# Performance work log

Measured on AMD Instinct MI355X. Metric: run time of the kernel, lower is better.

Reference implementation:

```python
import jax, jax.numpy as jnp
import numpy as np

S, B, T, H, K, FH, OUT = 4, 256, 256, 128, 5, 48, 1
DW, AW = 64, 32            # dynamics-MLP width, attention width
EPS_BN, EPS_U = 1e-5, 1e-6


def setup_inputs() -> dict:
    key = jax.random.key(0)
    ks = jax.random.split(key, 16)
    r = lambda i, shape, s: jax.random.normal(ks[i], shape, jnp.float32) * s
    return {
        "x": jax.random.normal(ks[0], (B, 1, T), jnp.float32),
        "t_span": jnp.linspace(0.0, 1.0, T, dtype=jnp.float32),
        # decomposer: per-scale DynamicDilationConv + BN + ReLU + Conv1d + BN + ReLU
        "c1w": r(1, (S, 1, 1, K), 0.3), "c1b": jnp.zeros((S, 1)),
        "bn1_g": jnp.ones((S, 1)), "bn1_b": jnp.zeros((S, 1)),
        "c2w": r(2, (S, 1, 1, K), 0.3), "c2b": jnp.zeros((S, 1)),
        "bn2_g": jnp.ones((S, 1)), "bn2_b": jnp.zeros((S, 1)),
        # per-scale ProbabilisticNeuralDynamics MLP: (H+1+1) -> 64 -> 2H
        "dw1": r(3, (S, H + 2, DW), 0.1), "db1": jnp.zeros((S, DW)),
        "dw2": r(4, (S, DW, 2 * H), 0.1), "db2": jnp.zeros((S, 2 * H)),
        # fusion attention H -> 32 -> 1
        "a1w": r(5, (H, AW), 0.1), "a1b": jnp.zeros((AW,)),
        "a2w": r(6, (AW, 1), 0.1), "a2b": jnp.zeros((1,)),
        # GRU (torch layout: W_ih [3H, in], W_hh [3H, H])
        "wih": r(7, (3 * H, OUT), 0.1), "whh": r(8, (3 * H, H), 0.05),
        "bih": jnp.zeros((3 * H,)), "bhh": jnp.zeros((3 * H,)),
        "fcw": r(9, (H, OUT), 0.1), "fcb": jnp.zeros((OUT,)),
        "lvw": r(10, (H, OUT), 0.1), "lvb": jnp.zeros((OUT,)),
        "init_token": jnp.zeros((1, OUT)),
    }


def _conv1d(x, w, b):
    # x:[B,C,L], w:[O,I,K]; dilation = round(clamp(exp(log_dilation=0),1)) = 1
    pad = (w.shape[-1] - 1) // 2
    y = jax.lax.conv_general_dilated(x, w, (1,), [(pad, pad)],
                                     dimension_numbers=("NCH", "OIH", "NCH"))
    return y + b[None, :, None]


def _bn(x, g, b):
    # BatchNorm1d in training mode: batch stats over (N, L)
    m = x.mean(axis=(0, 2), keepdims=True)
    v = x.var(axis=(0, 2), keepdims=True)
    return g[None, :, None] * (x - m) * jax.lax.rsqrt(v + EPS_BN) + b[None, :, None]


def _decompose(x, c1w, c1b, g1, b1, c2w, c2b, g2, b2):
    h = jnp.maximum(_bn(_conv1d(x, c1w, c1b), g1, b1), 0.0)
    h = jnp.maximum(_bn(_conv1d(h, c2w, c2b), g2, b2), 0.0)
    return h  # [B,1,T]


def _ode_scale(xseq, t_span, w1, b1, w2, b2):
    # xseq:[B,T,1]; integrate (mu, logvar) with RK4 on the t_span grid
    def f(t, h):
        idx = jnp.argmin(jnp.abs(t_span - t))
        x_t = jnp.take(xseq, idx, axis=1)                 # [B,1]
        tf = t * jnp.ones((h.shape[0], 1), h.dtype)       # time feature
        u = jnp.maximum(jnp.concatenate([h, x_t, tf], -1) @ w1 + b1, 0.0) @ w2 + b2
        return u[:, :H], u[:, H:]

    def step(carry, ts):
        h, lv = carry
        t0, t1 = ts
        dt = t1 - t0
        k1m, k1v = f(t0, h)
        k2m, k2v = f(t0 + dt / 2, h + dt / 2 * k1m)
        k3m, k3v = f(t0 + dt / 2, h + dt / 2 * k2m)
        k4m, k4v = f(t1, h + dt * k3m)
        h = h + dt / 6 * (k1m + 2 * k2m + 2 * k3m + k4m)
        lv = lv + dt / 6 * (k1v + 2 * k2v + 2 * k3v + k4v)
        return (h, lv), None

    z = jnp.zeros((xseq.shape[0], H), xseq.dtype)
    (h, lv), _ = jax.lax.scan(step, (z, z), (t_span[:-1], t_span[1:]))
    return h, lv  # final-time latent, matching h_sol[:, -1, :]


def _forward(x, t_span, c1w, c1b, bn1_g, bn1_b, c2w, c2b, bn2_g, bn2_b,
             dw1, db1, dw2, db2, a1w, a1b, a2w, a2b,
             wih, whh, bih, bhh, fcw, fcb, lvw, lvb, init_token):
    # multi-scale decomposition -> [S,B,1,T]
    comps = jax.vmap(_decompose, in_axes=(None, 0, 0, 0, 0, 0, 0, 0, 0))(
        x, c1w, c1b, bn1_g, bn1_b, c2w, c2b, bn2_g, bn2_b)
    xseqs = comps[:, :, 0, :, None]                       # [S,B,T,1]
    means, logvars = jax.vmap(_ode_scale, in_axes=(0, None, 0, 0, 0, 0))(
        xseqs, t_span, dw1, db1, dw2, db2)                # each [S,B,H]
    means = jnp.transpose(means, (1, 0, 2))               # [B,S,H]
    logvars = jnp.transpose(logvars, (1, 0, 2))
    # uncertainty-scaled attention fusion
    scores = jnp.maximum(means @ a1w + a1b, 0.0) @ a2w + a2b        # [B,S,1]
    uncert = jnp.mean(jnp.exp(logvars), axis=-1, keepdims=True)     # [B,S,1]
    weights = jax.nn.softmax(scores / (uncert + EPS_U), axis=1)
    fused = jnp.sum(weights * means, axis=1)              # [B,H]

    def dec_step(carry, _):
        h, tok = carry
        gi = tok @ wih.T + bih
        gh = h @ whh.T + bhh
        ir, iz, inn = jnp.split(gi, 3, axis=-1)
        hr, hz, hn = jnp.split(gh, 3, axis=-1)
        r = jax.nn.sigmoid(ir + hr)
        zz = jax.nn.sigmoid(iz + hz)
        n = jnp.tanh(inn + r * hn)
        h = (1.0 - zz) * n + zz * h
        pred = h @ fcw + fcb
        plv = h @ lvw + lvb
        return (h, pred), (pred, plv)

    tok0 = jnp.broadcast_to(init_token, (fused.shape[0], OUT))
    _, (outs, lvs) = jax.lax.scan(dec_step, (fused, tok0), None, length=FH)
    return jnp.transpose(outs, (1, 0, 2)), jnp.transpose(lvs, (1, 0, 2))


def reference(x, t_span, c1w, c1b, bn1_g, bn1_b, c2w, c2b, bn2_g, bn2_b,
              dw1, db1, dw2, db2, a1w, a1b, a2w, a2b,
              wih, whh, bih, bhh, fcw, fcb, lvw, lvb, init_token):
    return _forward(x, t_span, c1w, c1b, bn1_g, bn1_b, c2w, c2b, bn2_g, bn2_b,
                    dw1, db1, dw2, db2, a1w, a1b, a2w, a2b,
                    wih, whh, bih, bhh, fcw, fcb, lvw, lvb, init_token)
```

## Files before the change

### kernel.cpp

```cpp
#include <hip/hip_runtime.h>
#include <math.h>

#define NS   4
#define NB   256
#define NT   256
#define NH   128
#define NDW  64
#define NFH  48

__global__ __launch_bounds__(256) void k_d1(
    const float* __restrict__ x,
    const float* __restrict__ c1w, const float* __restrict__ c1b,
    float* __restrict__ tmpA, double* __restrict__ pp1)
{
    const int s     = blockIdx.x >> 6;
    const int chunk = blockIdx.x & 63;
    const int tid   = threadIdx.x;
    __shared__ double wred[4][2];

    float w[5];
#pragma unroll
    for (int k = 0; k < 5; ++k) w[k] = c1w[s*5 + k];
    const float cb = c1b[s];

    double ls = 0.0, lq = 0.0;
#pragma unroll
    for (int r = 0; r < 4; ++r) {
        const int bb = chunk*4 + r;
        const float* xb = x + bb*NT;
        float acc = cb;
#pragma unroll
        for (int k = 0; k < 5; ++k) {
            int tt = tid + k - 2;
            if (tt >= 0 && tt < NT) acc += xb[tt] * w[k];
        }
        tmpA[s*65536 + bb*NT + tid] = acc;
        ls += (double)acc; lq += (double)acc * (double)acc;
    }
#pragma unroll
    for (int off = 32; off > 0; off >>= 1) {
        ls += __shfl_xor(ls, off); lq += __shfl_xor(lq, off);
    }
    if ((tid & 63) == 0) { wred[tid>>6][0] = ls; wred[tid>>6][1] = lq; }
    __syncthreads();
    if (tid == 0) {
        pp1[(s*64 + chunk)*2 + 0] = wred[0][0]+wred[1][0]+wred[2][0]+wred[3][0];
        pp1[(s*64 + chunk)*2 + 1] = wred[0][1]+wred[1][1]+wred[2][1]+wred[3][1];
    }
}

__global__ __launch_bounds__(256) void k_d3(
    const float* __restrict__ tmpA, const double* __restrict__ pp1,
    const float* __restrict__ g1,  const float* __restrict__ b1,
    const float* __restrict__ c2w, const float* __restrict__ c2b,
    float* __restrict__ cv2, double* __restrict__ pp2)
{
    const int s     = blockIdx.x >> 6;
    const int chunk = blockIdx.x & 63;
    const int tid   = threadIdx.x;
    __shared__ float hsh[256];
    __shared__ double wred[4][2];

    double lsum = 0.0, lsq = 0.0;
    for (int q = 0; q < 64; ++q) {
        lsum += pp1[(s*64 + q)*2 + 0];
        lsq  += pp1[(s*64 + q)*2 + 1];
    }
    const double Nn = 65536.0;
    double mm = lsum / Nn;
    double vv = lsq / Nn - mm*mm;
    const float m1 = (float)mm, rs1 = (float)(1.0 / sqrt(vv + 1e-5));
    const float A1 = g1[s]*rs1, B1 = b1[s] - g1[s]*m1*rs1;

    float w[5];
#pragma unroll
    for (int k = 0; k < 5; ++k) w[k] = c2w[s*5 + k];
    const float cb = c2b[s];

    double ls = 0.0, lq = 0.0;
    for (int r = 0; r < 4; ++r) {
        const int bb = chunk*4 + r;
        float y = tmpA[s*65536 + bb*NT + tid];
        hsh[tid] = fmaxf(fmaf(A1, y, B1), 0.f);
        __syncthreads();
        float acc = cb;
#pragma unroll
        for (int k = 0; k < 5; ++k) {
            int tt = tid + k - 2;
            if (tt >= 0 && tt < NT) acc += hsh[tt] * w[k];
        }
        cv2[s*65536 + bb*NT + tid] = acc;
        ls += (double)acc; lq += (double)acc * (double)acc;
        __syncthreads();
    }
#pragma unroll
    for (int off = 32; off > 0; off >>= 1) {
        ls += __shfl_xor(ls, off); lq += __shfl_xor(lq, off);
    }
    if ((tid & 63) == 0) { wred[tid>>6][0] = ls; wred[tid>>6][1] = lq; }
    __syncthreads();
    if (tid == 0) {
        pp2[(s*64 + chunk)*2 + 0] = wred[0][0]+wred[1][0]+wred[2][0]+wred[3][0];
        pp2[(s*64 + chunk)*2 + 1] = wred[0][1]+wred[1][1]+wred[2][1]+wred[3][1];
    }
}

__global__ __launch_bounds__(64) void k_mat(
    const float* __restrict__ dw1, const float* __restrict__ dw2,
    const float* __restrict__ db2, const float* __restrict__ tspan,
    float* __restrict__ Mt, float* __restrict__ bM,
    int* __restrict__ imid_g, float* __restrict__ Tg)
{
    if (blockIdx.x == 256) {
        __shared__ float ts[256];
        const int t = threadIdx.x;
        for (int e = t; e < 256; e += 64) ts[e] = tspan[e];
        __syncthreads();
        for (int i = t; i < 255; i += 64) {
            float t0 = ts[i], t1 = ts[i+1];
            float tm = t0 + (t1 - t0) * 0.5f;
            int best = 0; float bd = fabsf(ts[0] - tm);
            for (int j = 1; j < 256; ++j) {
                float d = fabsf(ts[j] - tm);
                if (d < bd) { bd = d; best = j; }
            }
            imid_g[i] = best;
        }
        if (t == 0) {
            float T = 0.f;
            for (int i = 0; i < 255; ++i) T += (ts[i+1] - ts[i]);
            Tg[0] = T;
        }
        return;
    }
    const int s = blockIdx.x >> 6;
    const int c = blockIdx.x & 63;
    const int k = threadIdx.x;
    __shared__ float col[128];

    col[k]      = dw1[(s*130 + k)*64 + c];
    col[k + 64] = dw1[(s*130 + 64 + k)*64 + c];
    __syncthreads();

    const float4* dp = (const float4*)(dw2 + (s*64 + k)*256);
    double acc = 0.0;
#pragma unroll 8
    for (int j4 = 0; j4 < 32; ++j4) {
        float4 dv = dp[j4];
        acc += (double)dv.x * (double)col[4*j4+0]
             + (double)dv.y * (double)col[4*j4+1]
             + (double)dv.z * (double)col[4*j4+2]
             + (double)dv.w * (double)col[4*j4+3];
    }
    const int slot = (k & 48) | (((c & 15) - (k & 15)) & 15);
    Mt[(s*64 + c)*64 + slot] = (float)acc;

    double pb = (double)db2[s*256 + k]      * (double)col[k]
              + (double)db2[s*256 + 64 + k] * (double)col[k + 64];
#pragma unroll
    for (int off = 32; off > 0; off >>= 1) pb += __shfl_xor(pb, off);
    if (k == 0) bM[s*64 + c] = (float)pb;
}

__device__ __forceinline__ float rlf(float v, int l) {
    return __int_as_float(__builtin_amdgcn_readlane(__float_as_int(v), l));
}
__device__ __forceinline__ float pick4f(float r0, float r1, float r2, float r3, int i) {
    int l = i & 63, h = i >> 6;
    float a = (h & 2) ? ((h & 1) ? r3 : r2) : ((h & 1) ? r1 : r0);
    return rlf(a, l);
}
__device__ __forceinline__ float bperm(int addr, float v) {
    return __int_as_float(__builtin_amdgcn_ds_bpermute(addr, __float_as_int(v)));
}

#define FSTEP2(p) \
    asm("v_fmac_f32 %0, %1, %2 row_ror:" #p " row_mask:0xf bank_mask:0xf" \
        : "+v"(d0) : "v"(u0), "v"(McL[p])); \
    asm("v_fmac_f32 %0, %1, %2 row_ror:" #p " row_mask:0xf bank_mask:0xf" \
        : "+v"(d1) : "v"(u1v), "v"(McL[16+(p)]));

#define DOT(uin, vout) { \
    float u0 = bperm(A0, (uin)), u1v = bperm(A1, (uin)); \
    float d0 = fmaf(u0, McL[0], seed); \
    float d1 = u1v * McL[16]; \
    FSTEP2(1)  FSTEP2(2)  FSTEP2(3)  FSTEP2(4)  FSTEP2(5)  FSTEP2(6) \
    FSTEP2(7)  FSTEP2(8)  FSTEP2(9)  FSTEP2(10) FSTEP2(11) FSTEP2(12) \
    FSTEP2(13) FSTEP2(14) FSTEP2(15) \
    float part = d0 + d1; \
    pp[pb][w][l] = part; \
    __syncthreads(); \
    float oth = pp[pb][1 - w][l]; \
    vout = part + oth; \
    pb ^= 1; }

__global__ __attribute__((amdgpu_waves_per_eu(2)))
__launch_bounds__(128) void k_ode(
    const float* __restrict__ cv2, const double* __restrict__ pp2g,
    const float* __restrict__ g2,  const float* __restrict__ b2,
    const float* __restrict__ tspan, const int* __restrict__ imid_g,
    const float* __restrict__ Mt, const float* __restrict__ bM_g,
    const float* __restrict__ dw1, const float* __restrict__ db1,
    float* __restrict__ S_g)
{
    const int b   = blockIdx.x;
    const int s   = b >> 8;
    const int row = b & 255;
    const int tid = threadIdx.x;
    const int w   = tid >> 6;
    const int l   = tid & 63;

    __shared__ __align__(16) float xls[256];
    __shared__ __align__(16) float xms[256];
    __shared__ __align__(16) float pp[2][2][64];

    double lsum = 0.0, lsq = 0.0;
    for (int q = 0; q < 64; ++q) {
        lsum += pp2g[(s*64 + q)*2 + 0];
        lsq  += pp2g[(s*64 + q)*2 + 1];
    }
    const double Nn = 65536.0;
    double mmv = lsum / Nn;
    double vvv = lsq / Nn - mmv*mmv;
    const float m2 = (float)mmv, rs2 = (float)(1.0 / sqrt(vvv + 1e-5));
    const float bnA = g2[s]*rs2, bnB = b2[s] - g2[s]*m2*rs2;

    const float* __restrict__ xrow = cv2 + (s*NB + row)*NT;
    for (int e = tid; e < 256; e += 128)
        xls[e] = fmaxf(fmaf(bnA, xrow[e], bnB), 0.f);
    __syncthreads();
    for (int e = tid; e < 255; e += 128)
        xms[e] = xls[imid_g[e]];

    const float bMc = bM_g[s*64 + l];
    const float b1c = db1[s*64 + l];
    const float w1x = dw1[(s*130 + 128)*64 + l];
    const float w1t = dw1[(s*130 + 129)*64 + l];
    const float seed = (w == 0) ? bMc : 0.0f;

    float tr0 = tspan[l],       tr1 = tspan[64 + l];
    float tr2 = tspan[128 + l], tr3 = tspan[192 + l];

    float McL[32];
    const float4* mp = (const float4*)(Mt + (s*64 + l)*64 + 32*w);
#pragma unroll
    for (int j = 0; j < 8; ++j) {
        float4 t = mp[j];
        McL[4*j+0] = t.x; McL[4*j+1] = t.y; McL[4*j+2] = t.z; McL[4*j+3] = t.w;
    }
#pragma unroll
    for (int j = 0; j < 32; ++j) asm volatile("" : "+v"(McL[j]));

    const int lm = (l & 15) << 2;
    const int A0 = lm + 128*w;
    const int A1 = lm + 64 + 128*w;

    __syncthreads();

    float a = 0.f, S = 0.f;
    float t0  = rlf(tr0, 0);
    float t1  = rlf(tr0, 1);
    float xi  = xls[0], xmv = xms[0], x1v = xls[1];
    int   pb  = 0;

    for (int i = 0; i < 255; ++i) {
        float xin = 0.f, xmn = 0.f, x1n = 0.f, t1n = 0.f;
        if (i < 254) {
            xin = xls[i+1]; xmn = xms[i+1]; x1n = xls[i+2];
            t1n = pick4f(tr0, tr1, tr2, tr3, i + 2);
        }
        const float dt  = t1 - t0;
        const float tm  = t0 + dt * 0.5f;
        const float hdt = dt * 0.5f;
        const float c0  = b1c + xi*w1x  + t0*w1t;
        const float cm  = b1c + xmv*w1x + tm*w1t;
        const float c1  = b1c + x1v*w1x + t1*w1t;

        float u11 = fmaxf(a + c0, 0.f);
        float v1;  DOT(u11, v1)
        float u12 = fmaxf(fmaf(hdt, v1, a) + cm, 0.f);
        float v2;  DOT(u12, v2)
        float u13 = fmaxf(fmaf(hdt, v2, a) + cm, 0.f);
        float v3;  DOT(u13, v3)
        float u14 = fmaxf(fmaf(dt, v3, a) + c1, 0.f);
        float v4;  DOT(u14, v4)

        float d6 = dt * (1.0f / 6.0f);
        a += d6 * ((v1 + v4) + 2.f*(v2 + v3));
        S += d6 * ((u11 + u14) + 2.f*(u12 + u13));

        t0 = t1; t1 = t1n; xi = xin; xmv = xmn; x1v = x1n;
    }

    if (w == 0) S_g[(s*256 + row)*64 + l] = S;
}

__global__ __launch_bounds__(384, 1) void k_gru(
    const float* __restrict__ S_g, const float* __restrict__ dw2,
    const float* __restrict__ db2, const float* __restrict__ Tg,
    const float* __restrict__ a1w, const float* __restrict__ a1b,
    const float* __restrict__ a2w, const float* __restrict__ a2b,
    const float* __restrict__ wih, const float* __restrict__ whh,
    const float* __restrict__ bih, const float* __restrict__ bhh,
    const float* __restrict__ fcw, const float* __restrict__ fcb,
    const float* __restrict__ lvw, const float* __restrict__ lvb,
    const float* __restrict__ init_token, float* __restrict__ out)
{
    const int b   = blockIdx.x;
    const int tid = threadIdx.x;

    __shared__ __align__(16) float Ssh[4][64];
    __shared__ __align__(16) float msh[4][128];
    __shared__ __align__(16) float evs[4][128];
    __shared__ __align__(16) float hl[128];
    __shared__ float ghl[384];
    __shared__ float scoreL[4];
    __shared__ float unc_part[2][4];
    __shared__ float wgt[4];
    __shared__ float redL[2][2];
    __shared__ float tokL;

    if (tid < 256) {
        int s = tid >> 6, cc = tid & 63;
        Ssh[s][cc] = S_g[(s*256 + b)*64 + cc];
    }
    const float T = Tg[0];
    __syncthreads();

    for (int e = tid; e < 1024; e += 384) {
        int s = e >> 8, j = e & 255;
        float acc = T * db2[s*256 + j];
        const float4* s4 = (const float4*)Ssh[s];
#pragma unroll
        for (int k4 = 0; k4 < 16; ++k4) {
            float4 sv = s4[k4];
            acc += sv.x * dw2[(s*64 + 4*k4 + 0)*256 + j]
                 + sv.y * dw2[(s*64 + 4*k4 + 1)*256 + j]
                 + sv.z * dw2[(s*64 + 4*k4 + 2)*256 + j]
                 + sv.w * dw2[(s*64 + 4*k4 + 3)*256 + j];
        }
        if (j < 128) msh[s][j] = acc;
        else         evs[s][j - 128] = expf(acc);
    }
    __syncthreads();

    if (tid < 128) {
        int wv = tid >> 6;
#pragma unroll
        for (int s = 0; s < 4; ++s) {
            float v = evs[s][tid];
#pragma unroll
            for (int off = 32; off > 0; off >>= 1) v += __shfl_xor(v, off);
            if ((tid & 63) == 0) unc_part[wv][s] = v;
        }
    }
    if (tid < 128) {
        int s = tid >> 5, aq = tid & 31;
        float hd = a1b[aq];
#pragma unroll 4
        for (int i = 0; i < 128; ++i) hd += msh[s][i] * a1w[i*32 + aq];
        hd = fmaxf(hd, 0.f);
        float sc = hd * a2w[aq];
#pragma unroll
        for (int off = 16; off > 0; off >>= 1) sc += __shfl_xor(sc, off);
        if (aq == 0) scoreL[s] = sc + a2b[0];
    }
    __syncthreads();
    if (tid == 0) {
        float sv[4], mx = -1e30f;
#pragma unroll
        for (int s = 0; s < 4; ++s) {
            float u = (unc_part[0][s] + unc_part[1][s]) / 128.f;
            sv[s] = scoreL[s] / (u + 1e-6f);
            mx = fmaxf(mx, sv[s]);
        }
        float se = 0.f, ev[4];
#pragma unroll
        for (int s = 0; s < 4; ++s) { ev[s] = expf(sv[s] - mx); se += ev[s]; }
#pragma unroll
        for (int s = 0; s < 4; ++s) wgt[s] = ev[s] / se;
        tokL = init_token[0];
    }
    __syncthreads();
    if (tid < 128) {
        float f = 0.f;
#pragma unroll
        for (int s = 0; s < 4; ++s) f += wgt[s] * msh[s][tid];
        hl[tid] = f;
    }

    float4 whh4[32];
    const float4* wr = (const float4*)(whh + tid*128);
#pragma unroll
    for (int k = 0; k < 32; ++k) whh4[k] = wr[k];
    float bhhj = bhh[tid];
    float wih_r = 0.f, wih_z = 0.f, wih_n = 0.f;
    float bih_r = 0.f, bih_z = 0.f, bih_n = 0.f;
    float fcwi = 0.f, lvwi = 0.f;
    if (tid < 128) {
        wih_r = wih[tid]; wih_z = wih[128+tid]; wih_n = wih[256+tid];
        bih_r = bih[tid]; bih_z = bih[128+tid]; bih_n = bih[256+tid];
        fcwi  = fcw[tid]; lvwi  = lvw[tid];
    }
    const float fcbv = fcb[0], lvbv = lvb[0];
    __syncthreads();

    for (int t = 0; t < NFH; ++t) {
        float g0 = 0.f, g1 = 0.f, g2 = 0.f, g3 = 0.f;
        const float4* h4 = (const float4*)hl;
#pragma unroll
        for (int k = 0; k < 32; ++k) {
            float4 hv = h4[k];
            float4 wvv = whh4[k];
            g0 += hv.x * wvv.x; g1 += hv.y * wvv.y;
            g2 += hv.z * wvv.z; g3 += hv.w * wvv.w;
        }
        ghl[tid] = ((g0 + g1) + (g2 + g3)) + bhhj;
        __syncthreads();

        if (tid < 128) {
            float tok = tokL;
            float r  = 1.f / (1.f + expf(-(tok*wih_r + bih_r + ghl[tid])));
            float zz = 1.f / (1.f + expf(-(tok*wih_z + bih_z + ghl[128+tid])));
            float n  = tanhf(tok*wih_n + bih_n + r * ghl[256+tid]);
            float hn = (1.f - zz) * n + zz * hl[tid];
            hl[tid] = hn;
            float pg = hn * fcwi, pl = hn * lvwi;
#pragma unroll
            for (int off = 32; off > 0; off >>= 1) {
                pg += __shfl_xor(pg, off);
                pl += __shfl_xor(pl, off);
            }
            int wvx = tid >> 6;
            if ((tid & 63) == 0) { redL[wvx][0] = pg; redL[wvx][1] = pl; }
        }
        __syncthreads();
        if (tid == 0) {
            float pr = redL[0][0] + redL[1][0] + fcbv;
            float pv = redL[0][1] + redL[1][1] + lvbv;
            out[b*NFH + t] = pr;
            out[NB*NFH + b*NFH + t] = pv;
            tokL = pr;
        }
        __syncthreads();
    }
}

extern "C" void kernel_launch(void* const* d_in, const int* in_sizes, int n_in,
                              void* d_out, int out_size, void* d_ws, size_t ws_size,
                              hipStream_t stream)
{
    const float* x      = (const float*)d_in[0];
    const float* tspan  = (const float*)d_in[1];
    const float* c1w    = (const float*)d_in[2];
    const float* c1b    = (const float*)d_in[3];
    const float* bn1g   = (const float*)d_in[4];
    const float* bn1b   = (const float*)d_in[5];
    const float* c2w    = (const float*)d_in[6];
    const float* c2b    = (const float*)d_in[7];
    const float* bn2g   = (const float*)d_in[8];
    const float* bn2b   = (const float*)d_in[9];
    const float* dw1    = (const float*)d_in[10];
    const float* db1    = (const float*)d_in[11];
    const float* dw2    = (const float*)d_in[12];
    const float* db2    = (const float*)d_in[13];
    const float* a1w    = (const float*)d_in[14];
    const float* a1b    = (const float*)d_in[15];
    const float* a2w    = (const float*)d_in[16];
    const float* a2b    = (const float*)d_in[17];
    const float* wih    = (const float*)d_in[18];
    const float* whh    = (const float*)d_in[19];
    const float* bih    = (const float*)d_in[20];
    const float* bhh    = (const float*)d_in[21];
    const float* fcw    = (const float*)d_in[22];
    const float* fcb    = (const float*)d_in[23];
    const float* lvw    = (const float*)d_in[24];
    const float* lvb    = (const float*)d_in[25];
    const float* itok   = (const float*)d_in[26];

    float* ws    = (float*)d_ws;
    float*  cv2  = ws;
    float*  tmpA = ws + 262144;
    float*  S_g  = ws + 524288;
    float*  Mt   = ws + 589824;
    float*  bMg  = ws + 606208;
    float*  Tg   = ws + 606464;
    int*    imid = (int*)(ws + 606720);
    double* pp1  = (double*)(ws + 606976);
    double* pp2  = (double*)(ws + 608000);

    k_d1<<<256, 256, 0, stream>>>(x, c1w, c1b, tmpA, pp1);
    k_mat<<<257, 64, 0, stream>>>(dw1, dw2, db2, tspan, Mt, bMg, imid, Tg);
    k_d3<<<256, 256, 0, stream>>>(tmpA, pp1, bn1g, bn1b, c2w, c2b, cv2, pp2);
    k_ode<<<1024, 128, 0, stream>>>(cv2, pp2, bn2g, bn2b, tspan, imid,
                                    Mt, bMg, dw1, db1, S_g);
    k_gru<<<256, 384, 0, stream>>>(S_g, dw2, db2, Tg, a1w, a1b, a2w, a2b,
                                   wih, whh, bih, bhh, fcw, fcb, lvw, lvb,
                                   itok, (float*)d_out);
}
```

Baseline: 406.3 us.

## Split ODE matvec reduction across four waves instead of two

Doubles the k_ode block to 256 threads, so each wave handles a 16-element slice of the 64-wide inner dimension instead of 32. Each wave then runs one bpermute and 16 DPP FMAs per dot instead of two bpermutes and 32 FMAs, which shortens the serial per-step latency of the sequential ODE loop. Partials are stored as a [64][4] LDS array and summed with one float4 read. The trade-off is twice as many waves per block competing for CU slots, and a barrier across four waves at every dot.

```diff
diff --git a/kernel.cpp b/kernel.cpp
--- a/kernel.cpp
+++ b/kernel.cpp
@@ -174,28 +174,27 @@
     return __int_as_float(__builtin_amdgcn_ds_bpermute(addr, __float_as_int(v)));
 }
 
-#define FSTEP2(p) \
-    asm("v_fmac_f32 %0, %1, %2 row_ror:" #p " row_mask:0xf bank_mask:0xf" \
-        : "+v"(d0) : "v"(u0), "v"(McL[p])); \
-    asm("v_fmac_f32 %0, %1, %2 row_ror:" #p " row_mask:0xf bank_mask:0xf" \
-        : "+v"(d1) : "v"(u1v), "v"(McL[16+(p)]));
+#define KSTEP(pe, po) \
+    asm("v_fmac_f32 %0, %1, %2 row_ror:" #pe " row_mask:0xf bank_mask:0xf" \
+        : "+v"(d_e) : "v"(ug), "v"(McL[pe])); \
+    asm("v_fmac_f32 %0, %1, %2 row_ror:" #po " row_mask:0xf bank_mask:0xf" \
+        : "+v"(d_o) : "v"(ug), "v"(McL[po]));
 
 #define DOT(uin, vout) { \
-    float u0 = bperm(A0, (uin)), u1v = bperm(A1, (uin)); \
-    float d0 = fmaf(u0, McL[0], seed); \
-    float d1 = u1v * McL[16]; \
-    FSTEP2(1)  FSTEP2(2)  FSTEP2(3)  FSTEP2(4)  FSTEP2(5)  FSTEP2(6) \
-    FSTEP2(7)  FSTEP2(8)  FSTEP2(9)  FSTEP2(10) FSTEP2(11) FSTEP2(12) \
-    FSTEP2(13) FSTEP2(14) FSTEP2(15) \
-    float part = d0 + d1; \
-    pp[pb][w][l] = part; \
+    float ug = bperm(A, (uin)); \
+    float d_e = fmaf(ug, McL[0], seed); \
+    float d_o; \
+    asm("v_mul_f32 %0, %1, %2 row_ror:1 row_mask:0xf bank_mask:0xf" \
+        : "=v"(d_o) : "v"(ug), "v"(McL[1])); \
+    KSTEP(2,3)   KSTEP(4,5)   KSTEP(6,7)   KSTEP(8,9) \
+    KSTEP(10,11) KSTEP(12,13) KSTEP(14,15) \
+    pps[pb][l][w] = d_e + d_o; \
     __syncthreads(); \
-    float oth = pp[pb][1 - w][l]; \
-    vout = part + oth; \
+    float4 pv = *(const float4*)&pps[pb][l][0]; \
+    vout = (pv.x + pv.y) + (pv.z + pv.w); \
     pb ^= 1; }
 
-__global__ __attribute__((amdgpu_waves_per_eu(2)))
-__launch_bounds__(128) void k_ode(
+__global__ __launch_bounds__(256, 4) void k_ode(
     const float* __restrict__ cv2, const double* __restrict__ pp2g,
     const float* __restrict__ g2,  const float* __restrict__ b2,
     const float* __restrict__ tspan, const int* __restrict__ imid_g,
@@ -212,7 +211,7 @@
 
     __shared__ __align__(16) float xls[256];
     __shared__ __align__(16) float xms[256];
-    __shared__ __align__(16) float pp[2][2][64];
+    __shared__ __align__(16) float pps[2][64][4];
 
     double lsum = 0.0, lsq = 0.0;
     for (int q = 0; q < 64; ++q) {
@@ -226,11 +225,9 @@
     const float bnA = g2[s]*rs2, bnB = b2[s] - g2[s]*m2*rs2;
 
     const float* __restrict__ xrow = cv2 + (s*NB + row)*NT;
-    for (int e = tid; e < 256; e += 128)
-        xls[e] = fmaxf(fmaf(bnA, xrow[e], bnB), 0.f);
-    __syncthreads();
-    for (int e = tid; e < 255; e += 128)
-        xms[e] = xls[imid_g[e]];
+    if (tid < 256) xls[tid] = fmaxf(fmaf(bnA, xrow[tid], bnB), 0.f);
+    __syncthreads();
+    if (tid < 255) xms[tid] = xls[imid_g[tid]];
 
     const float bMc = bM_g[s*64 + l];
     const float b1c = db1[s*64 + l];
@@ -241,19 +238,17 @@
     float tr0 = tspan[l],       tr1 = tspan[64 + l];
     float tr2 = tspan[128 + l], tr3 = tspan[192 + l];
 
-    float McL[32];
-    const float4* mp = (const float4*)(Mt + (s*64 + l)*64 + 32*w);
-#pragma unroll
-    for (int j = 0; j < 8; ++j) {
+    float McL[16];
+    const float4* mp = (const float4*)(Mt + (s*64 + l)*64 + 16*w);
+#pragma unroll
+    for (int j = 0; j < 4; ++j) {
         float4 t = mp[j];
         McL[4*j+0] = t.x; McL[4*j+1] = t.y; McL[4*j+2] = t.z; McL[4*j+3] = t.w;
     }
 #pragma unroll
-    for (int j = 0; j < 32; ++j) asm volatile("" : "+v"(McL[j]));
-
-    const int lm = (l & 15) << 2;
-    const int A0 = lm + 128*w;
-    const int A1 = lm + 64 + 128*w;
+    for (int j = 0; j < 16; ++j) asm volatile("" : "+v"(McL[j]));
+
+    const int A = ((l & 15) << 2) + (w << 6);
 
     __syncthreads();
 
@@ -492,7 +487,7 @@
     k_d1<<<256, 256, 0, stream>>>(x, c1w, c1b, tmpA, pp1);
     k_mat<<<257, 64, 0, stream>>>(dw1, dw2, db2, tspan, Mt, bMg, imid, Tg);
     k_d3<<<256, 256, 0, stream>>>(tmpA, pp1, bn1g, bn1b, c2w, c2b, cv2, pp2);
-    k_ode<<<1024, 128, 0, stream>>>(cv2, pp2, bn2g, bn2b, tspan, imid,
+    k_ode<<<1024, 256, 0, stream>>>(cv2, pp2, bn2g, bn2b, tspan, imid,
                                     Mt, bMg, dw1, db1, S_g);
     k_gru<<<256, 384, 0, stream>>>(S_g, dw2, db2, Tg, a1w, a1b, a2w, a2b,
                                    wih, whh, bih, bhh, fcw, fcb, lvw, lvb,
```

After: 431.1 us. 6.1% more time.
